# Kernel optimization log

Measured on AMD Instinct MI355X. Metric: run time of the kernel, lower is better.

## Reference

```python
import jax, jax.numpy as jnp
import numpy as np

B, S, D, H = 2, 2048, 1024, 16
HD = D // H  # 64

def setup_inputs() -> dict:
    key = jax.random.key(0)
    ks = jax.random.split(key, 6)
    s = 1.0 / np.sqrt(D)
    return {
        "x": jax.random.normal(ks[0], (B, S, D), dtype=jnp.float32),
        "wq": jax.random.normal(ks[1], (D, D), dtype=jnp.float32) * s,
        "wk": jax.random.normal(ks[2], (D, D), dtype=jnp.float32) * s,
        "wv": jax.random.normal(ks[3], (D, D), dtype=jnp.float32) * s,
        "wo": jax.random.normal(ks[4], (D, D), dtype=jnp.float32) * s,
        "bo": jax.random.normal(ks[5], (D,), dtype=jnp.float32) * 0.01,
    }

def reference(x, wq, wk, wv, wo, bo):
    b, s, _ = x.shape
    # QKV projections (qkvBias=False), reshape to [b, h, s, hd]
    q = (x @ wq).reshape(b, s, H, HD).transpose(0, 2, 1, 3)
    k = (x @ wk).reshape(b, s, H, HD).transpose(0, 2, 1, 3)
    v = (x @ wv).reshape(b, s, H, HD).transpose(0, 2, 1, 3)
    # scores, causal mask (upper triangle -> -inf), scale, softmax
    scores = jnp.einsum('bhqd,bhkd->bhqk', q, k)
    causal = jnp.triu(jnp.ones((s, s), dtype=bool), k=1)
    scores = jnp.where(causal, -jnp.inf, scores) / np.sqrt(HD)
    weights = jax.nn.softmax(scores, axis=-1)  # dropout=0 (eval)
    ctx = jnp.einsum('bhqk,bhkd->bhqd', weights, v)
    ctx = ctx.transpose(0, 2, 1, 3).reshape(b, s, D)
    return ctx @ wo + bo
```

## Files before the change

### kernel.cpp

```cpp
#include <hip/hip_runtime.h>
#include <hip/hip_bf16.h>
#include <math.h>

#define BB 2
#define SS 2048
#define DD 1024
#define HH 16
#define HDIM 64

typedef unsigned short u16;
typedef __attribute__((ext_vector_type(8))) short bfrag;
typedef __attribute__((ext_vector_type(4))) float f32x4;

#define NEG_BIG (-1e30f)
#define QSCALE 0.18033688011112042f

__device__ __forceinline__ u16 f2u(float f) {
    unsigned int u = __builtin_bit_cast(unsigned int, f);
    u += 0x7fffu + ((u >> 16) & 1u);
    return (u16)(u >> 16);
}

__device__ __forceinline__ void async16(const u16* g, u16* l) {
    __builtin_amdgcn_global_load_lds((__attribute__((address_space(1))) void*)g,
                                     (__attribute__((address_space(3))) void*)l,
                                     16, 0, 0);
}

__device__ __forceinline__ f32x4 mfma16(bfrag a, bfrag b, f32x4 c) {
    return __builtin_amdgcn_mfma_f32_16x16x32_bf16(a, b, c, 0, 0, 0);
}

__global__ __launch_bounds__(256) void cvt_x_k(const float* __restrict__ x,
                                               u16* __restrict__ xb) {
    int i = (blockIdx.x * 256 + threadIdx.x) * 8;
    float4 a = *(const float4*)(x + i);
    float4 b = *(const float4*)(x + i + 4);
    u16 o[8] = { f2u(a.x), f2u(a.y), f2u(a.z), f2u(a.w),
                 f2u(b.x), f2u(b.y), f2u(b.z), f2u(b.w) };
    *(uint4*)(xb + i) = *(uint4*)o;
}

__global__ __launch_bounds__(256) void cvt_wT_k(const float* __restrict__ wq,
                                                const float* __restrict__ wk,
                                                const float* __restrict__ wv,
                                                const float* __restrict__ wo,
                                                u16* __restrict__ wT) {
    const float* w = (blockIdx.z == 0) ? wq : (blockIdx.z == 1) ? wk
                   : (blockIdx.z == 2) ? wv : wo;
    u16* o = wT + (size_t)blockIdx.z * DD * DD;
    __shared__ __align__(16) u16 T[64][72];
    const int t = threadIdx.x;
    const int k0 = blockIdx.x * 64, n0 = blockIdx.y * 64;
    {
        int kr = t >> 2, nb = (t & 3) * 16;
        const float4* s4 = (const float4*)(w + (size_t)(k0 + kr) * DD + n0 + nb);
        #pragma unroll
        for (int jj = 0; jj < 4; ++jj) {
            float4 v = s4[jj];
            T[kr][nb + jj*4 + 0] = f2u(v.x);
            T[kr][nb + jj*4 + 1] = f2u(v.y);
            T[kr][nb + jj*4 + 2] = f2u(v.z);
            T[kr][nb + jj*4 + 3] = f2u(v.w);
        }
    }
    __syncthreads();
    {
        int nr = t >> 2, kb = (t & 3) * 16;
        u16 tmp[16];
        #pragma unroll
        for (int j = 0; j < 16; ++j) tmp[j] = T[kb + j][nr];
        *(uint4*)(o + (size_t)(n0 + nr) * DD + k0 + kb)     = ((uint4*)tmp)[0];
        *(uint4*)(o + (size_t)(n0 + nr) * DD + k0 + kb + 8) = ((uint4*)tmp)[1];
    }
}

__global__ __launch_bounds__(256) void gemm_qkv_k(
    const u16* __restrict__ xb, const u16* __restrict__ wT,
    u16* __restrict__ Qo, u16* __restrict__ Ko, u16* __restrict__ Vt)
{
    const u16* wTz = wT + (size_t)blockIdx.z * DD * DD;
    const float osc = (blockIdx.z == 0) ? QSCALE : 1.0f;

    __shared__ __align__(16) u16 smem[8192];
    u16* As = smem;
    u16* Bs = smem + 4096;

    const int t = threadIdx.x;
    const int m0 = blockIdx.x * 128, n0 = blockIdx.y * 128;
    const int lane15 = t & 15, quad = (t >> 4) & 3, wave = t >> 6;
    const int wm = wave & 1, wn = wave >> 1;

    const int ar0 = t >> 2,        as0 = t & 3;
    const int ar1 = (t + 256) >> 2, as1 = (t + 256) & 3;
    const int ac0 = as0 ^ ((ar0 >> 1) & 3);
    const int ac1 = as1 ^ ((ar1 >> 1) & 3);
    const u16* gA0 = xb  + (size_t)(m0 + ar0) * DD + ac0 * 8;
    const u16* gA1 = xb  + (size_t)(m0 + ar1) * DD + ac1 * 8;
    const u16* gB0 = wTz + (size_t)(n0 + ar0) * DD + ac0 * 8;
    const u16* gB1 = wTz + (size_t)(n0 + ar1) * DD + ac1 * 8;
    u16* lA0 = As + (t & 192) * 8;  u16* lA1 = As + (t & 192) * 8 + 2048;
    u16* lB0 = Bs + (t & 192) * 8;  u16* lB1 = Bs + (t & 192) * 8 + 2048;

    int aoff[4], boff[4];
    #pragma unroll
    for (int mi = 0; mi < 4; ++mi) {
        int r = wm * 64 + mi * 16 + lane15;
        aoff[mi] = (r * 4 + (quad ^ ((r >> 1) & 3))) * 8;
    }
    #pragma unroll
    for (int ni = 0; ni < 4; ++ni) {
        int r = wn * 64 + ni * 16 + lane15;
        boff[ni] = (r * 4 + (quad ^ ((r >> 1) & 3))) * 8;
    }

    f32x4 acc[4][4];
    #pragma unroll
    for (int mi = 0; mi < 4; ++mi)
        #pragma unroll
        for (int ni = 0; ni < 4; ++ni)
            acc[mi][ni] = (f32x4){0.f, 0.f, 0.f, 0.f};

    for (int k0 = 0; k0 < DD; k0 += 32) {
        async16(gA0 + k0, lA0);
        async16(gA1 + k0, lA1);
        async16(gB0 + k0, lB0);
        async16(gB1 + k0, lB1);
        __syncthreads();
        bfrag av[4], bv[4];
        #pragma unroll
        for (int mi = 0; mi < 4; ++mi) av[mi] = *(const bfrag*)(As + aoff[mi]);
        #pragma unroll
        for (int ni = 0; ni < 4; ++ni) bv[ni] = *(const bfrag*)(Bs + boff[ni]);
        #pragma unroll
        for (int mi = 0; mi < 4; ++mi)
            #pragma unroll
            for (int ni = 0; ni < 4; ++ni)
                acc[mi][ni] = mfma16(av[mi], bv[ni], acc[mi][ni]);
        __syncthreads();
    }

    if (blockIdx.z != 2) {
        u16* out = (blockIdx.z == 0) ? Qo : Ko;
        #pragma unroll
        for (int mi = 0; mi < 4; ++mi) {
            #pragma unroll
            for (int r = 0; r < 4; ++r) {
                int m = m0 + wm * 64 + mi * 16 + quad * 4 + r;
                int b = m >> 11, s = m & (SS - 1);
                #pragma unroll
                for (int ni = 0; ni < 4; ++ni) {
                    int n = n0 + wn * 64 + ni * 16 + lane15;
                    int h = n >> 6, hd = n & 63;
                    out[(((size_t)(b * HH + h)) * SS + s) * HDIM + hd] = f2u(acc[mi][ni][r] * osc);
                }
            }
        }
    } else {
        u16* T = smem;
        const int bq = m0 >> 11;
        const int ms = m0 & (SS - 1);
        #pragma unroll
        for (int hh = 0; hh < 2; ++hh) {
            if (wn == hh) {
                #pragma unroll
                for (int mi = 0; mi < 4; ++mi)
                    #pragma unroll
                    for (int r = 0; r < 4; ++r) {
                        int ml = wm * 64 + mi * 16 + quad * 4 + r;
                        #pragma unroll
                        for (int ni = 0; ni < 4; ++ni) {
                            int nl = ni * 16 + lane15;
                            T[nl * 128 + (ml ^ ((nl & 7) << 4))] = f2u(acc[mi][ni][r]);
                        }
                    }
            }
            __syncthreads();
            const int h = (n0 >> 6) + hh;
            u16* dst = Vt + ((size_t)(bq * HH + h)) * (HDIM * SS);
            #pragma unroll
            for (int i = 0; i < 4; ++i) {
                int c = t + i * 256;
                int row = c >> 4;
                int mb  = (c & 15) * 8;
                uint4 val = *(const uint4*)&T[row * 128 + (mb ^ ((row & 7) << 4))];
                *(uint4*)(dst + (size_t)row * SS + ms + mb) = val;
            }
            __syncthreads();
        }
    }
}

__global__ __launch_bounds__(256) void gemm_out_k(
    const u16* __restrict__ ctxb, const u16* __restrict__ woT,
    const float* __restrict__ bo, float* __restrict__ out)
{
    __shared__ __align__(16) u16 As[128 * 32];
    __shared__ __align__(16) u16 Bs[64 * 32];

    const int t = threadIdx.x;
    const int m0 = blockIdx.x * 128, n0 = blockIdx.y * 64;
    const int lane15 = t & 15, quad = (t >> 4) & 3, wave = t >> 6;
    const int wm = wave & 1, wn = wave >> 1;

    const int ar0 = t >> 2,        as0 = t & 3;
    const int ar1 = (t + 256) >> 2, as1 = (t + 256) & 3;
    const int ac0 = as0 ^ ((ar0 >> 1) & 3);
    const int ac1 = as1 ^ ((ar1 >> 1) & 3);
    const u16* gA0 = ctxb + (size_t)(m0 + ar0) * DD + ac0 * 8;
    const u16* gA1 = ctxb + (size_t)(m0 + ar1) * DD + ac1 * 8;
    const u16* gB0 = woT  + (size_t)(n0 + ar0) * DD + ac0 * 8;
    u16* lA0 = As + (t & 192) * 8;  u16* lA1 = As + (t & 192) * 8 + 2048;
    u16* lB0 = Bs + (t & 192) * 8;

    int aoff[4], boff[2];
    #pragma unroll
    for (int mi = 0; mi < 4; ++mi) {
        int r = wm * 64 + mi * 16 + lane15;
        aoff[mi] = (r * 4 + (quad ^ ((r >> 1) & 3))) * 8;
    }
    #pragma unroll
    for (int ni = 0; ni < 2; ++ni) {
        int r = wn * 32 + ni * 16 + lane15;
        boff[ni] = (r * 4 + (quad ^ ((r >> 1) & 3))) * 8;
    }

    f32x4 acc[4][2];
    #pragma unroll
    for (int mi = 0; mi < 4; ++mi)
        #pragma unroll
        for (int ni = 0; ni < 2; ++ni)
            acc[mi][ni] = (f32x4){0.f, 0.f, 0.f, 0.f};

    for (int k0 = 0; k0 < DD; k0 += 32) {
        async16(gA0 + k0, lA0);
        async16(gA1 + k0, lA1);
        async16(gB0 + k0, lB0);
        __syncthreads();
        bfrag av[4], bv[2];
        #pragma unroll
        for (int mi = 0; mi < 4; ++mi) av[mi] = *(const bfrag*)(As + aoff[mi]);
        #pragma unroll
        for (int ni = 0; ni < 2; ++ni) bv[ni] = *(const bfrag*)(Bs + boff[ni]);
        #pragma unroll
        for (int mi = 0; mi < 4; ++mi)
            #pragma unroll
            for (int ni = 0; ni < 2; ++ni)
                acc[mi][ni] = mfma16(av[mi], bv[ni], acc[mi][ni]);
        __syncthreads();
    }

    float bias[2];
    #pragma unroll
    for (int ni = 0; ni < 2; ++ni)
        bias[ni] = bo[n0 + wn * 32 + ni * 16 + lane15];

    #pragma unroll
    for (int mi = 0; mi < 4; ++mi) {
        #pragma unroll
        for (int r = 0; r < 4; ++r) {
            int m = m0 + wm * 64 + mi * 16 + quad * 4 + r;
            #pragma unroll
            for (int ni = 0; ni < 2; ++ni) {
                int n = n0 + wn * 32 + ni * 16 + lane15;
                out[(size_t)m * DD + n] = acc[mi][ni][r] + bias[ni];
            }
        }
    }
}

__global__ __launch_bounds__(256, 4) void attn_k(
    const u16* __restrict__ Q, const u16* __restrict__ K,
    const u16* __restrict__ Vt, u16* __restrict__ ctx)
{
    __shared__ __align__(16) u16 QP[64 * 64];
    __shared__ __align__(16) u16 Ks[2][64 * 64];
    __shared__ __align__(16) u16 Vs[2][64 * 64];

    const int t = threadIdx.x;
    const int lane15 = t & 15, quad = (t >> 4) & 3, wave = t >> 6;
    const int bh = blockIdx.x;
    const int qt = (int)(gridDim.y - 1) - (int)blockIdx.y;
    const int q0 = qt * 64;
    const int b = bh >> 4, h = bh & 15;

    const u16* Qb = Q  + (size_t)bh * SS * HDIM;
    const u16* Kb = K  + (size_t)bh * SS * HDIM;
    const u16* Vb = Vt + (size_t)bh * HDIM * SS;

    const int kr0 = t >> 3,         ks0 = t & 7;
    const int kr1 = (t + 256) >> 3, ks1 = (t + 256) & 7;
    const int kc0 = ks0 ^ (kr0 & 7);
    const int kc1 = ks1 ^ (kr1 & 7);
    const int ldst = (t & 192) * 8;

    async16(Qb + (size_t)(q0 + kr0) * HDIM + kc0 * 8, QP + ldst);
    async16(Qb + (size_t)(q0 + kr1) * HDIM + kc1 * 8, QP + ldst + 2048);
    async16(Kb + (size_t)kr0 * HDIM + kc0 * 8, Ks[0] + ldst);
    async16(Kb + (size_t)kr1 * HDIM + kc1 * 8, Ks[0] + ldst + 2048);
    async16(Vb + (size_t)kr0 * SS + kc0 * 8, Vs[0] + ldst);
    async16(Vb + (size_t)kr1 * SS + kc1 * 8, Vs[0] + ldst + 2048);

    const int qrow = wave * 16 + lane15;
    int qoff[2], koff[4][2];
    #pragma unroll
    for (int kh = 0; kh < 2; ++kh)
        qoff[kh] = (qrow * 8 + ((kh * 4 + quad) ^ (qrow & 7))) * 8;
    #pragma unroll
    for (int ni = 0; ni < 4; ++ni)
        #pragma unroll
        for (int kh = 0; kh < 2; ++kh) {
            int row = ni * 16 + lane15;
            koff[ni][kh] = (row * 8 + ((kh * 4 + quad) ^ (row & 7))) * 8;
        }

    __syncthreads();
    bfrag aq[2];
    aq[0] = *(const bfrag*)(QP + qoff[0]);
    aq[1] = *(const bfrag*)(QP + qoff[1]);
    __syncthreads();

    f32x4 acc_o[4];
    float rsum[4] = {0.f, 0.f, 0.f, 0.f};
    #pragma unroll
    for (int nd = 0; nd < 4; ++nd) acc_o[nd] = (f32x4){0.f, 0.f, 0.f, 0.f};

    const int qgb = q0 + wave * 16 + quad * 4;

    for (int kt = 0; kt <= qt; ++kt) {
        if (kt < qt) {
            const int nv0 = (kt + 1) * 64;
            u16* kd = Ks[(kt + 1) & 1];
            u16* vd = Vs[(kt + 1) & 1];
            async16(Kb + (size_t)(nv0 + kr0) * HDIM + kc0 * 8, kd + ldst);
            async16(Kb + (size_t)(nv0 + kr1) * HDIM + kc1 * 8, kd + ldst + 2048);
            async16(Vb + (size_t)kr0 * SS + nv0 + kc0 * 8, vd + ldst);
            async16(Vb + (size_t)kr1 * SS + nv0 + kc1 * 8, vd + ldst + 2048);
        }
        const u16* ksb = Ks[kt & 1];
        const u16* vsb = Vs[kt & 1];
        const int kv0 = kt * 64;

        f32x4 s_acc[4];
        #pragma unroll
        for (int ni = 0; ni < 4; ++ni) s_acc[ni] = (f32x4){0.f, 0.f, 0.f, 0.f};
        #pragma unroll
        for (int kh = 0; kh < 2; ++kh)
            #pragma unroll
            for (int ni = 0; ni < 4; ++ni)
                s_acc[ni] = mfma16(aq[kh], *(const bfrag*)(ksb + koff[ni][kh]), s_acc[ni]);

        const bool diag = (kt == qt);
        #pragma unroll
        for (int ni = 0; ni < 4; ++ni) {
            int kvg = kv0 + ni * 16 + lane15;
            #pragma unroll
            for (int r = 0; r < 4; ++r) {
                float v = s_acc[ni][r];
                if (diag && (kvg > qgb + r)) v = NEG_BIG;
                float pw = exp2f(v);
                unsigned pu = __builtin_bit_cast(unsigned, pw);
                rsum[r] += __builtin_bit_cast(float, pu & 0xffff0000u);
                int row = wave * 16 + quad * 4 + r;
                int col = ni * 16 + lane15;
                QP[(row * 8 + ((col >> 3) ^ (row & 7))) * 8 + (col & 7)] = (u16)(pu >> 16);
            }
        }

        #pragma unroll
        for (int kh = 0; kh < 2; ++kh) {
            bfrag ap = *(const bfrag*)(QP + qoff[kh]);
            #pragma unroll
            for (int nd = 0; nd < 4; ++nd)
                acc_o[nd] = mfma16(ap, *(const bfrag*)(vsb + koff[nd][kh]), acc_o[nd]);
        }
        __syncthreads();
    }

    #pragma unroll
    for (int off = 1; off < 16; off <<= 1)
        #pragma unroll
        for (int r = 0; r < 4; ++r)
            rsum[r] += __shfl_xor(rsum[r], off, 64);

    #pragma unroll
    for (int r = 0; r < 4; ++r) {
        float inv = 1.f / rsum[r];
        int srow = q0 + wave * 16 + quad * 4 + r;
        size_t base = ((size_t)b * SS + srow) * DD + h * HDIM;
        #pragma unroll
        for (int nd = 0; nd < 4; ++nd)
            ctx[base + nd * 16 + lane15] = f2u(acc_o[nd][r] * inv);
    }
}

extern "C" void kernel_launch(void* const* d_in, const int* in_sizes, int n_in,
                              void* d_out, int out_size, void* d_ws, size_t ws_size,
                              hipStream_t stream) {
    const float* x  = (const float*)d_in[0];
    const float* wq = (const float*)d_in[1];
    const float* wk = (const float*)d_in[2];
    const float* wv = (const float*)d_in[3];
    const float* wo = (const float*)d_in[4];
    const float* bo = (const float*)d_in[5];
    float* out = (float*)d_out;

    char* ws = (char*)d_ws;
    const size_t MB8 = (size_t)8 * 1024 * 1024;
    u16* xb  = (u16*)(ws);
    u16* wT  = (u16*)(ws + MB8);
    u16* Qb  = (u16*)(ws + 2 * MB8);
    u16* Kb  = (u16*)(ws + 3 * MB8);
    u16* Vt  = (u16*)(ws + 4 * MB8);
    u16* ctxb = xb;

    cvt_x_k <<<2048, 256, 0, stream>>>(x, xb);
    cvt_wT_k<<<dim3(16, 16, 4), 256, 0, stream>>>(wq, wk, wv, wo, wT);
    gemm_qkv_k<<<dim3(32, 8, 3), 256, 0, stream>>>(xb, wT, Qb, Kb, Vt);
    attn_k  <<<dim3(32, 32), 256, 0, stream>>>(Qb, Kb, Vt, ctxb);
    gemm_out_k<<<dim3(32, 16), 256, 0, stream>>>(ctxb, wT + (size_t)3 * DD * DD, bo, out);
}
```

Measured before the change: 187.0 us.

## Double-buffer GEMM K-loop LDS tiles and merge conversion kernels into one launch

New measurement: 195.4 us. +4.5%, slower.

```diff
diff --git a/kernel.cpp b/kernel.cpp
--- a/kernel.cpp
+++ b/kernel.cpp
@@ -31,27 +31,30 @@
     return __builtin_amdgcn_mfma_f32_16x16x32_bf16(a, b, c, 0, 0, 0);
 }
 
-__global__ __launch_bounds__(256) void cvt_x_k(const float* __restrict__ x,
-                                               u16* __restrict__ xb) {
-    int i = (blockIdx.x * 256 + threadIdx.x) * 8;
-    float4 a = *(const float4*)(x + i);
-    float4 b = *(const float4*)(x + i + 4);
-    u16 o[8] = { f2u(a.x), f2u(a.y), f2u(a.z), f2u(a.w),
-                 f2u(b.x), f2u(b.y), f2u(b.z), f2u(b.w) };
-    *(uint4*)(xb + i) = *(uint4*)o;
-}
-
-__global__ __launch_bounds__(256) void cvt_wT_k(const float* __restrict__ wq,
-                                                const float* __restrict__ wk,
-                                                const float* __restrict__ wv,
-                                                const float* __restrict__ wo,
-                                                u16* __restrict__ wT) {
-    const float* w = (blockIdx.z == 0) ? wq : (blockIdx.z == 1) ? wk
-                   : (blockIdx.z == 2) ? wv : wo;
-    u16* o = wT + (size_t)blockIdx.z * DD * DD;
+__global__ __launch_bounds__(256) void prep_k(
+    const float* __restrict__ x,  u16* __restrict__ xb,
+    const float* __restrict__ wq, const float* __restrict__ wk,
+    const float* __restrict__ wv, const float* __restrict__ wo,
+    u16* __restrict__ wT)
+{
+    const int id = blockIdx.x;
+    const int t = threadIdx.x;
+    if (id < 2048) {
+        int i = (id * 256 + t) * 8;
+        float4 a = *(const float4*)(x + i);
+        float4 b = *(const float4*)(x + i + 4);
+        u16 o[8] = { f2u(a.x), f2u(a.y), f2u(a.z), f2u(a.w),
+                     f2u(b.x), f2u(b.y), f2u(b.z), f2u(b.w) };
+        *(uint4*)(xb + i) = *(uint4*)o;
+        return;
+    }
+    const int wid = id - 2048;
+    const int z = wid >> 8;
+    const int kt = wid & 15, nt = (wid >> 4) & 15;
+    const float* w = (z == 0) ? wq : (z == 1) ? wk : (z == 2) ? wv : wo;
+    u16* o = wT + (size_t)z * DD * DD;
     __shared__ __align__(16) u16 T[64][72];
-    const int t = threadIdx.x;
-    const int k0 = blockIdx.x * 64, n0 = blockIdx.y * 64;
+    const int k0 = kt * 64, n0 = nt * 64;
     {
         int kr = t >> 2, nb = (t & 3) * 16;
         const float4* s4 = (const float4*)(w + (size_t)(k0 + kr) * DD + n0 + nb);
@@ -82,9 +85,8 @@
     const u16* wTz = wT + (size_t)blockIdx.z * DD * DD;
     const float osc = (blockIdx.z == 0) ? QSCALE : 1.0f;
 
-    __shared__ __align__(16) u16 smem[8192];
-    u16* As = smem;
-    u16* Bs = smem + 4096;
+    __shared__ __align__(16) u16 As[2][4096];
+    __shared__ __align__(16) u16 Bs[2][4096];
 
     const int t = threadIdx.x;
     const int m0 = blockIdx.x * 128, n0 = blockIdx.y * 128;
@@ -99,8 +101,7 @@
     const u16* gA1 = xb  + (size_t)(m0 + ar1) * DD + ac1 * 8;
     const u16* gB0 = wTz + (size_t)(n0 + ar0) * DD + ac0 * 8;
     const u16* gB1 = wTz + (size_t)(n0 + ar1) * DD + ac1 * 8;
-    u16* lA0 = As + (t & 192) * 8;  u16* lA1 = As + (t & 192) * 8 + 2048;
-    u16* lB0 = Bs + (t & 192) * 8;  u16* lB1 = Bs + (t & 192) * 8 + 2048;
+    const int ldst = (t & 192) * 8;
 
     int aoff[4], boff[4];
     #pragma unroll
@@ -121,23 +122,31 @@
         for (int ni = 0; ni < 4; ++ni)
             acc[mi][ni] = (f32x4){0.f, 0.f, 0.f, 0.f};
 
-    for (int k0 = 0; k0 < DD; k0 += 32) {
-        async16(gA0 + k0, lA0);
-        async16(gA1 + k0, lA1);
-        async16(gB0 + k0, lB0);
-        async16(gB1 + k0, lB1);
+    async16(gA0, &As[0][ldst]);
+    async16(gA1, &As[0][ldst + 2048]);
+    async16(gB0, &Bs[0][ldst]);
+    async16(gB1, &Bs[0][ldst + 2048]);
+
+    for (int it = 0; it < 32; ++it) {
         __syncthreads();
+        const int cb = it & 1, nb = cb ^ 1;
+        if (it < 31) {
+            const int nk = (it + 1) * 32;
+            async16(gA0 + nk, &As[nb][ldst]);
+            async16(gA1 + nk, &As[nb][ldst + 2048]);
+            async16(gB0 + nk, &Bs[nb][ldst]);
+            async16(gB1 + nk, &Bs[nb][ldst + 2048]);
+        }
         bfrag av[4], bv[4];
         #pragma unroll
-        for (int mi = 0; mi < 4; ++mi) av[mi] = *(const bfrag*)(As + aoff[mi]);
-        #pragma unroll
-        for (int ni = 0; ni < 4; ++ni) bv[ni] = *(const bfrag*)(Bs + boff[ni]);
+        for (int mi = 0; mi < 4; ++mi) av[mi] = *(const bfrag*)&As[cb][aoff[mi]];
+        #pragma unroll
+        for (int ni = 0; ni < 4; ++ni) bv[ni] = *(const bfrag*)&Bs[cb][boff[ni]];
         #pragma unroll
         for (int mi = 0; mi < 4; ++mi)
             #pragma unroll
             for (int ni = 0; ni < 4; ++ni)
                 acc[mi][ni] = mfma16(av[mi], bv[ni], acc[mi][ni]);
-        __syncthreads();
     }
 
     if (blockIdx.z != 2) {
@@ -157,7 +166,8 @@
             }
         }
     } else {
-        u16* T = smem;
+        __syncthreads();
+        u16* T = &As[0][0];
         const int bq = m0 >> 11;
         const int ms = m0 & (SS - 1);
         #pragma unroll
@@ -195,8 +205,8 @@
     const u16* __restrict__ ctxb, const u16* __restrict__ woT,
     const float* __restrict__ bo, float* __restrict__ out)
 {
-    __shared__ __align__(16) u16 As[128 * 32];
-    __shared__ __align__(16) u16 Bs[64 * 32];
+    __shared__ __align__(16) u16 As[2][4096];
+    __shared__ __align__(16) u16 Bs[2][2048];
 
     const int t = threadIdx.x;
     const int m0 = blockIdx.x * 128, n0 = blockIdx.y * 64;
@@ -210,8 +220,7 @@
     const u16* gA0 = ctxb + (size_t)(m0 + ar0) * DD + ac0 * 8;
     const u16* gA1 = ctxb + (size_t)(m0 + ar1) * DD + ac1 * 8;
     const u16* gB0 = woT  + (size_t)(n0 + ar0) * DD + ac0 * 8;
-    u16* lA0 = As + (t & 192) * 8;  u16* lA1 = As + (t & 192) * 8 + 2048;
-    u16* lB0 = Bs + (t & 192) * 8;
+    const int ldst = (t & 192) * 8;
 
     int aoff[4], boff[2];
     #pragma unroll
@@ -232,22 +241,29 @@
         for (int ni = 0; ni < 2; ++ni)
             acc[mi][ni] = (f32x4){0.f, 0.f, 0.f, 0.f};
 
-    for (int k0 = 0; k0 < DD; k0 += 32) {
-        async16(gA0 + k0, lA0);
-        async16(gA1 + k0, lA1);
-        async16(gB0 + k0, lB0);
+    async16(gA0, &As[0][ldst]);
+    async16(gA1, &As[0][ldst + 2048]);
+    async16(gB0, &Bs[0][ldst]);
+
+    for (int it = 0; it < 32; ++it) {
         __syncthreads();
+        const int cb = it & 1, nb = cb ^ 1;
+        if (it < 31) {
+            const int nk = (it + 1) * 32;
+            async16(gA0 + nk, &As[nb][ldst]);
+            async16(gA1 + nk, &As[nb][ldst + 2048]);
+            async16(gB0 + nk, &Bs[nb][ldst]);
+        }
         bfrag av[4], bv[2];
         #pragma unroll
-        for (int mi = 0; mi < 4; ++mi) av[mi] = *(const bfrag*)(As + aoff[mi]);
-        #pragma unroll
-        for (int ni = 0; ni < 2; ++ni) bv[ni] = *(const bfrag*)(Bs + boff[ni]);
+        for (int mi = 0; mi < 4; ++mi) av[mi] = *(const bfrag*)&As[cb][aoff[mi]];
+        #pragma unroll
+        for (int ni = 0; ni < 2; ++ni) bv[ni] = *(const bfrag*)&Bs[cb][boff[ni]];
         #pragma unroll
         for (int mi = 0; mi < 4; ++mi)
             #pragma unroll
             for (int ni = 0; ni < 2; ++ni)
                 acc[mi][ni] = mfma16(av[mi], bv[ni], acc[mi][ni]);
-        __syncthreads();
     }
 
     float bias[2];
@@ -296,10 +312,10 @@
 
     async16(Qb + (size_t)(q0 + kr0) * HDIM + kc0 * 8, QP + ldst);
     async16(Qb + (size_t)(q0 + kr1) * HDIM + kc1 * 8, QP + ldst + 2048);
-    async16(Kb + (size_t)kr0 * HDIM + kc0 * 8, Ks[0] + ldst);
-    async16(Kb + (size_t)kr1 * HDIM + kc1 * 8, Ks[0] + ldst + 2048);
-    async16(Vb + (size_t)kr0 * SS + kc0 * 8, Vs[0] + ldst);
-    async16(Vb + (size_t)kr1 * SS + kc1 * 8, Vs[0] + ldst + 2048);
+    async16(Kb + (size_t)kr0 * HDIM + kc0 * 8, &Ks[0][ldst]);
+    async16(Kb + (size_t)kr1 * HDIM + kc1 * 8, &Ks[0][ldst + 2048]);
+    async16(Vb + (size_t)kr0 * SS + kc0 * 8, &Vs[0][ldst]);
+    async16(Vb + (size_t)kr1 * SS + kc1 * 8, &Vs[0][ldst + 2048]);
 
     const int qrow = wave * 16 + lane15;
     int qoff[2], koff[4][2];
@@ -330,15 +346,13 @@
     for (int kt = 0; kt <= qt; ++kt) {
         if (kt < qt) {
             const int nv0 = (kt + 1) * 64;
-            u16* kd = Ks[(kt + 1) & 1];
-            u16* vd = Vs[(kt + 1) & 1];
-            async16(Kb + (size_t)(nv0 + kr0) * HDIM + kc0 * 8, kd + ldst);
-            async16(Kb + (size_t)(nv0 + kr1) * HDIM + kc1 * 8, kd + ldst + 2048);
-            async16(Vb + (size_t)kr0 * SS + nv0 + kc0 * 8, vd + ldst);
-            async16(Vb + (size_t)kr1 * SS + nv0 + kc1 * 8, vd + ldst + 2048);
-        }
-        const u16* ksb = Ks[kt & 1];
-        const u16* vsb = Vs[kt & 1];
+            const int pb = (kt + 1) & 1;
+            async16(Kb + (size_t)(nv0 + kr0) * HDIM + kc0 * 8, &Ks[pb][ldst]);
+            async16(Kb + (size_t)(nv0 + kr1) * HDIM + kc1 * 8, &Ks[pb][ldst + 2048]);
+            async16(Vb + (size_t)kr0 * SS + nv0 + kc0 * 8, &Vs[pb][ldst]);
+            async16(Vb + (size_t)kr1 * SS + nv0 + kc1 * 8, &Vs[pb][ldst + 2048]);
+        }
+        const int cb = kt & 1;
         const int kv0 = kt * 64;
 
         f32x4 s_acc[4];
@@ -348,7 +362,7 @@
         for (int kh = 0; kh < 2; ++kh)
             #pragma unroll
             for (int ni = 0; ni < 4; ++ni)
-                s_acc[ni] = mfma16(aq[kh], *(const bfrag*)(ksb + koff[ni][kh]), s_acc[ni]);
+                s_acc[ni] = mfma16(aq[kh], *(const bfrag*)&Ks[cb][koff[ni][kh]], s_acc[ni]);
 
         const bool diag = (kt == qt);
         #pragma unroll
@@ -372,7 +386,7 @@
             bfrag ap = *(const bfrag*)(QP + qoff[kh]);
             #pragma unroll
             for (int nd = 0; nd < 4; ++nd)
-                acc_o[nd] = mfma16(ap, *(const bfrag*)(vsb + koff[nd][kh]), acc_o[nd]);
+                acc_o[nd] = mfma16(ap, *(const bfrag*)&Vs[cb][koff[nd][kh]], acc_o[nd]);
         }
         __syncthreads();
     }
@@ -414,8 +428,7 @@
     u16* Vt  = (u16*)(ws + 4 * MB8);
     u16* ctxb = xb;
 
-    cvt_x_k <<<2048, 256, 0, stream>>>(x, xb);
-    cvt_wT_k<<<dim3(16, 16, 4), 256, 0, stream>>>(wq, wk, wv, wo, wT);
+    prep_k  <<<3072, 256, 0, stream>>>(x, xb, wq, wk, wv, wo, wT);
     gemm_qkv_k<<<dim3(32, 8, 3), 256, 0, stream>>>(xb, wT, Qb, Kb, Vt);
     attn_k  <<<dim3(32, 32), 256, 0, stream>>>(Qb, Kb, Vt, ctxb);
     gemm_out_k<<<dim3(32, 16), 256, 0, stream>>>(ctxb, wT + (size_t)3 * DD * DD, bo, out);
```
